# Performance work log

Measured on AMD Instinct MI355X. Metric: run time of the kernel, lower is better.

## Reference

```python
import jax, jax.numpy as jnp
import numpy as np

N, M = 100000, 12          # atoms, neighbors per atom
ORIG, F, NBR, H = 92, 64, 41, 128
NC = 3                     # n_conv
C = 3125                   # crystals
EPS = 1e-5                 # BatchNorm eps (torch default)


def setup_inputs() -> dict:
    key = jax.random.key(0)
    ks = jax.random.split(key, 8)
    w = lambda k, s: jax.random.normal(k, s, jnp.float32) * 0.05
    return {
        "atom_fea": jax.random.normal(ks[0], (N, ORIG), jnp.float32),
        "nbr_fea": jax.random.normal(ks[1], (N, M, NBR), jnp.float32),
        "nbr_fea_idx": jax.random.randint(ks[2], (N, M), 0, N),
        "seg_ids": jnp.sort(jax.random.randint(ks[3], (N,), 0, C)),
        "n_crystals": C,
        "mask": jnp.ones((ORIG,), jnp.float32),
        "embW": w(ks[4], (ORIG, F)), "embb": jnp.zeros((F,), jnp.float32),
        "fcW": w(ks[5], (NC, 2 * F + NBR, 2 * F)), "fcb": jnp.zeros((NC, 2 * F), jnp.float32),
        "bn1g": jnp.ones((NC, 2 * F), jnp.float32), "bn1b": jnp.zeros((NC, 2 * F), jnp.float32),
        "bn2g": jnp.ones((NC, F), jnp.float32), "bn2b": jnp.zeros((NC, F), jnp.float32),
        "c2fW": w(ks[6], (F, H)), "c2fb": jnp.zeros((H,), jnp.float32),
        "outW": w(ks[7], (H, 1)), "outb": jnp.zeros((1,), jnp.float32),
    }


def _bn(x, g, b):
    # BatchNorm1d in training mode: biased batch stats over dim 0
    mu = x.mean(0)
    var = x.var(0)
    return (x - mu) * jax.lax.rsqrt(var + EPS) * g + b


def reference(atom_fea, nbr_fea, nbr_fea_idx, seg_ids, n_crystals, mask,
              embW, embb, fcW, fcb, bn1g, bn1b, bn2g, bn2b,
              c2fW, c2fb, outW, outb):
    x = (atom_fea * mask) @ embW + embb              # [N, F]
    for l in range(NC):                              # fixed small layer loop
        nbr = x[nbr_fea_idx]                         # [N, M, F] gather
        self_f = jnp.broadcast_to(x[:, None, :], (N, M, F))
        tot = jnp.concatenate([self_f, nbr, nbr_fea], axis=-1)   # [N, M, 2F+NBR]
        g = tot @ fcW[l] + fcb[l]                    # [N, M, 2F]
        g = _bn(g.reshape(N * M, 2 * F), bn1g[l], bn1b[l]).reshape(N, M, 2 * F)
        filt, core = g[..., :F], g[..., F:]
        summed = jnp.sum(jax.nn.sigmoid(filt) * jax.nn.softplus(core), axis=1)  # [N, F]
        x = jax.nn.softplus(x + _bn(summed, bn2g[l], bn2b[l]))
    # per-crystal mean pooling (segment ids replace list of index maps)
    sums = jax.ops.segment_sum(x, seg_ids, num_segments=n_crystals)
    cnt = jax.ops.segment_sum(jnp.ones((N,), x.dtype), seg_ids, num_segments=n_crystals)
    crys = sums / jnp.maximum(cnt, 1.0)[:, None]     # [C, F]
    crys = jax.nn.softplus(jax.nn.softplus(crys) @ c2fW + c2fb)  # [C, H]
    return crys @ outW + outb                        # [C, 1]
```

## Files before the change

kernel.cpp:

```cpp
#include <hip/hip_runtime.h>
#include <hip/hip_bf16.h>


#define NN    100000
#define MM    12
#define ORIG  92
#define FF    64
#define NBR   41
#define HH    128
#define NCONV 3
#define CC    3125
#define K2    169
#define GG    128
#define EPSV  1e-5f

#define TILE_ATOMS 8
#define TILE_ROWS  96
#define NTILES     (NN / TILE_ATOMS)
#define SLOTS      24
#define WPK_L      (48 * 64 * 8)
#define CONV_GRID  1024
#define ETILES     1563
#define PCHUNK_ROWS 128
#define PCHUNK_F32  (PCHUNK_ROWS * NBR)
#define PCHUNK_U4   (PCHUNK_F32 / 4)
#define NPCHUNK     ((NN * MM) / PCHUNK_ROWS)
#define LOG2E_F    1.44269504088896341f
#define LN2_F      0.69314718055994531f

typedef __attribute__((ext_vector_type(8))) short bf16x8;
typedef __attribute__((ext_vector_type(4))) float f32x4;

__device__ __forceinline__ float softplusf(float v) {
    return fmaxf(v, 0.f) + log1pf(expf(-fabsf(v)));
}
__device__ __forceinline__ float sigmoidf_(float v) {
    return 1.f / (1.f + expf(-v));
}
__device__ __forceinline__ ushort f2bf(float f) {
    __hip_bfloat16 h = __float2bfloat16(f);
    return *(ushort*)&h;
}
__device__ __forceinline__ float bf2f(ushort h) {
    uint u = ((uint)h) << 16;
    return __uint_as_float(u);
}
__device__ __forceinline__ void gload_lds16(const void* gsrc, void* ldst) {
    __builtin_amdgcn_global_load_lds(
        (const __attribute__((address_space(1))) unsigned int*)gsrc,
        (__attribute__((address_space(3))) unsigned int*)ldst, 16, 0, 0);
}

__global__ void packWemb_kernel(const float* __restrict__ embW, const float* __restrict__ mask,
                                ushort* __restrict__ wemb) {
    int b = blockIdx.x;
    int cf = b / 3;
    int kk = b - cf * 3;
    int lane = threadIdx.x;
    int c = cf * 16 + (lane & 15);
#pragma unroll
    for (int i = 0; i < 8; i++) {
        int k = kk * 32 + (lane >> 4) * 8 + i;
        float v = (k < ORIG) ? mask[k] * embW[k * FF + c] : 0.f;
        wemb[((size_t)b * 64 + lane) * 8 + i] = f2bf(v);
    }
}

__launch_bounds__(256)
__global__ void embed_mfma(const float* __restrict__ af, const ushort* __restrict__ wemb,
                           const float* __restrict__ embb,
                           float* __restrict__ x, ushort* __restrict__ xb) {
    __shared__ __align__(16) ushort Ae[64 * 128];
    const int t = threadIdx.x;
    const int lane = t & 63;
    const int w = t >> 6;
    const int l15 = lane & 15;
    const int lg = lane >> 4;
    const int a0 = blockIdx.x * 64;

    bf16x8 bfrag[4][3];
#pragma unroll
    for (int cf = 0; cf < 4; cf++)
#pragma unroll
        for (int kk = 0; kk < 3; kk++)
            bfrag[cf][kk] = *(const bf16x8*)&wemb[(((size_t)(cf * 3 + kk)) * 64 + lane) * 8];

#pragma unroll
    for (int uu = 0; uu < 3; uu++) {
        int u = uu * 256 + t;
        int row = u / 12;
        int slot = u - row * 12;
        int a = a0 + row;
        if (a >= NN) a = NN - 1;
        const float* src = af + (size_t)a * ORIG + slot * 8;
        float v[8];
        float4 p0 = *(const float4*)src;
        v[0] = p0.x; v[1] = p0.y; v[2] = p0.z; v[3] = p0.w;
        if (slot < 11) {
            float4 p1 = *(const float4*)(src + 4);
            v[4] = p1.x; v[5] = p1.y; v[6] = p1.z; v[7] = p1.w;
        } else {
            v[4] = v[5] = v[6] = v[7] = 0.f;
        }
        uint4 val;
        val.x = (uint)f2bf(v[0]) | ((uint)f2bf(v[1]) << 16);
        val.y = (uint)f2bf(v[2]) | ((uint)f2bf(v[3]) << 16);
        val.z = (uint)f2bf(v[4]) | ((uint)f2bf(v[5]) << 16);
        val.w = (uint)f2bf(v[6]) | ((uint)f2bf(v[7]) << 16);
        *(uint4*)&Ae[row * 128 + ((slot ^ (row & 7)) * 8)] = val;
    }
    __syncthreads();

    f32x4 acc[4];
#pragma unroll
    for (int cf = 0; cf < 4; cf++) acc[cf] = (f32x4){0.f, 0.f, 0.f, 0.f};

#pragma unroll
    for (int kk = 0; kk < 3; kk++) {
        int row = w * 16 + l15;
        int slot = kk * 4 + lg;
        bf16x8 a = *(const bf16x8*)&Ae[row * 128 + ((slot ^ (row & 7)) * 8)];
#pragma unroll
        for (int cf = 0; cf < 4; cf++)
            acc[cf] = __builtin_amdgcn_mfma_f32_16x16x32_bf16(a, bfrag[cf][kk], acc[cf], 0, 0, 0);
    }

#pragma unroll
    for (int cf = 0; cf < 4; cf++) {
        int c = cf * 16 + l15;
        float bb = embb[c];
#pragma unroll
        for (int q = 0; q < 4; q++) {
            int a = a0 + w * 16 + lg * 4 + q;
            if (a < NN) {
                float v = acc[cf][q] + bb;
                x[(size_t)a * FF + c] = v;
                xb[(size_t)a * FF + c] = f2bf(v);
            }
        }
    }
}

__global__ void packW_kernel(const float* __restrict__ fcW, ushort* __restrict__ wpk) {
    int b = blockIdx.x;
    int l = b / 48;
    int r = b - l * 48;
    int cf = r / 6;
    int kk = r - cf * 6;
    int lane = threadIdx.x;
    int c = cf * 16 + (lane & 15);
#pragma unroll
    for (int i = 0; i < 8; i++) {
        int k = kk * 32 + (lane >> 4) * 8 + i;
        float v = (k < K2) ? fcW[(l * K2 + k) * GG + c] : 0.f;
        wpk[((size_t)b * 64 + lane) * 8 + i] = f2bf(v);
    }
}

__launch_bounds__(256)
__global__ void prepack_nbr(const float* __restrict__ nbr_fea, ushort* __restrict__ nbrb) {
    __shared__ float buf[PCHUNK_F32];
    const int t = threadIdx.x;
    for (int chunk = blockIdx.x; chunk < NPCHUNK; chunk += gridDim.x) {
        const uint4* src = (const uint4*)(nbr_fea + (size_t)chunk * PCHUNK_F32);
        __syncthreads();
#pragma unroll
        for (int i = 0; i < 6; i++) {
            int u = i * 256 + t;
            if (u < PCHUNK_U4) *(uint4*)&buf[u * 4] = src[u];
        }
        __syncthreads();
#pragma unroll
        for (int i = 0; i < 4; i++) {
            int u = i * 256 + t;
            int row = u >> 3;
            int kb = (u & 7) * 8;
            ushort h[8];
#pragma unroll
            for (int j = 0; j < 8; j++)
                h[j] = (kb + j < NBR) ? f2bf(buf[row * NBR + kb + j]) : (ushort)0;
            uint4 val;
            val.x = (uint)h[0] | ((uint)h[1] << 16);
            val.y = (uint)h[2] | ((uint)h[3] << 16);
            val.z = (uint)h[4] | ((uint)h[5] << 16);
            val.w = (uint)h[6] | ((uint)h[7] << 16);
            *(uint4*)&nbrb[((size_t)chunk * PCHUNK_ROWS + row) * 64 + kb] = val;
        }
    }
}

template <int MODE>
__launch_bounds__(256, 3)
__global__ void conv_fused(const ushort* __restrict__ xb, const ushort* __restrict__ nbrb,
                           const int* __restrict__ nidx, const ushort* __restrict__ wpk_l,
                           const float* __restrict__ fcb_l,
                           float* __restrict__ stats,
                           const float* __restrict__ sc1, const float* __restrict__ sh1,
                           float* __restrict__ summed, float* __restrict__ stats2) {
    __shared__ __align__(16) ushort As[3][TILE_ROWS * 64];
    __shared__ int nbstage[2][TILE_ROWS];
    __shared__ float red[256];

    const int t = threadIdx.x;
    const int lane = t & 63;
    const int w = t >> 6;
    const int l15 = lane & 15;
    const int lg = lane >> 4;

    bf16x8 bfrag[2][6];
#pragma unroll
    for (int c2 = 0; c2 < 2; c2++)
#pragma unroll
        for (int kk = 0; kk < 6; kk++)
            bfrag[c2][kk] = *(const bf16x8*)&wpk_l[((((w + 4 * c2) * 6 + kk) * 64 + lane) * 8)];

    const int chF = w * 16 + l15;
    float scF = 0.f, shF = 0.f, scC = 0.f, shC = 0.f;
    if (MODE == 1) {
        scF = sc1[chF]; shF = sh1[chF];
        scC = sc1[chF + 64]; shC = sh1[chF + 64];
    }

    float sAF = 0.f, sBF = 0.f, sAC = 0.f, sBC = 0.f;
    float s2a = 0.f, s2b = 0.f;

    int pt = t; if (pt >= TILE_ROWS) pt -= TILE_ROWS; if (pt >= TILE_ROWS) pt -= TILE_ROWS;
    const int pidx = (pt & 7) * MM + (pt >> 3);

    int rowi[3], sli[3];
#pragma unroll
    for (int i = 0; i < 3; i++) {
        int u = w * 192 + i * 64 + lane;
        rowi[i] = u >> 3;
        sli[i] = (u & 7) ^ (rowi[i] & 7);
    }
    const ushort* p0p[3];
    const ushort* p2p[3];
#pragma unroll
    for (int i = 0; i < 3; i++) {
        p0p[i] = xb + ((size_t)blockIdx.x * TILE_ATOMS + (rowi[i] & 7)) * 64 + sli[i] * 8;
        p2p[i] = nbrb + ((size_t)blockIdx.x * TILE_ROWS + (rowi[i] & 7) * MM + (rowi[i] >> 3)) * 64
                 + sli[i] * 8;
    }
    const size_t st0 = (size_t)CONV_GRID * TILE_ATOMS * 64;
    const size_t st2 = (size_t)CONV_GRID * TILE_ROWS * 64;

    auto issue0 = [&]() {
#pragma unroll
        for (int i = 0; i < 3; i++) {
            gload_lds16(p0p[i], &As[0][(w * 192 + i * 64) * 8]);
            p0p[i] += st0;
        }
    };
    auto issue1 = [&](int nb) {
#pragma unroll
        for (int i = 0; i < 3; i++)
            gload_lds16(xb + (size_t)nbstage[nb][rowi[i]] * 64 + sli[i] * 8,
                        &As[1][(w * 192 + i * 64) * 8]);
    };
    auto issue2 = [&]() {
#pragma unroll
        for (int i = 0; i < 3; i++) {
            gload_lds16(p2p[i], &As[2][(w * 192 + i * 64) * 8]);
            p2p[i] += st2;
        }
    };

    int tile = blockIdx.x;
    int idx_cur;
    {
        int nx0 = nidx[tile * TILE_ROWS + pidx];
        int nx1 = nidx[(tile + CONV_GRID) * TILE_ROWS + pidx];
        if (t < TILE_ROWS) { nbstage[0][t] = nx0; nbstage[1][t] = nx1; }
        __syncthreads();
        idx_cur = nidx[(tile + 2 * CONV_GRID) * TILE_ROWS + pidx];
        issue0(); issue1(0); issue2();
        asm volatile("" ::: "memory");
    }

    for (int it = 0; tile < NTILES; tile += CONV_GRID, ++it) {
        const bool have1 = (tile + CONV_GRID)     < NTILES;
        const bool have2 = (tile + 2 * CONV_GRID) < NTILES;
        const bool have3 = (tile + 3 * CONV_GRID) < NTILES;

        int idx_next = 0;
        if (have3) idx_next = nidx[(tile + 3 * CONV_GRID) * TILE_ROWS + pidx];

        f32x4 acc[6][2];
#pragma unroll
        for (int rf = 0; rf < 6; rf++)
#pragma unroll
            for (int c2 = 0; c2 < 2; c2++) acc[rf][c2] = (f32x4){0.f, 0.f, 0.f, 0.f};

        if (it == 0)       { asm volatile("s_waitcnt vmcnt(7)"  ::: "memory"); }
        else if (have3) {
            if (MODE == 1) { asm volatile("s_waitcnt vmcnt(11)" ::: "memory"); }
            else           { asm volatile("s_waitcnt vmcnt(7)"  ::: "memory"); }
        } else {
            if (MODE == 1) { asm volatile("s_waitcnt vmcnt(10)" ::: "memory"); }
            else           { asm volatile("s_waitcnt vmcnt(6)"  ::: "memory"); }
        }
        __builtin_amdgcn_s_barrier();
        __builtin_amdgcn_sched_barrier(0);
#pragma unroll
        for (int kx = 0; kx < 2; kx++) {
            int kk = kx;
#pragma unroll
            for (int rf = 0; rf < 6; rf++) {
                int row = rf * 16 + l15;
                int s8r = kx * 4 + lg;
                bf16x8 a = *(const bf16x8*)&As[0][row * 64 + ((s8r ^ (row & 7)) * 8)];
                acc[rf][0] = __builtin_amdgcn_mfma_f32_16x16x32_bf16(a, bfrag[0][kk], acc[rf][0], 0, 0, 0);
                acc[rf][1] = __builtin_amdgcn_mfma_f32_16x16x32_bf16(a, bfrag[1][kk], acc[rf][1], 0, 0, 0);
            }
        }
        asm volatile("" ::: "memory");
        __builtin_amdgcn_s_barrier();
        if (have1) issue0();
        asm volatile("" ::: "memory");

        if (it == 0)       { asm volatile("s_waitcnt vmcnt(7)"  ::: "memory"); }
        else if (!have1) {
            if (MODE == 1) { asm volatile("s_waitcnt vmcnt(7)"  ::: "memory"); }
            else           { asm volatile("s_waitcnt vmcnt(3)"  ::: "memory"); }
        } else if (have3) {
            if (MODE == 1) { asm volatile("s_waitcnt vmcnt(11)" ::: "memory"); }
            else           { asm volatile("s_waitcnt vmcnt(7)"  ::: "memory"); }
        } else {
            if (MODE == 1) { asm volatile("s_waitcnt vmcnt(10)" ::: "memory"); }
            else           { asm volatile("s_waitcnt vmcnt(6)"  ::: "memory"); }
        }
        __builtin_amdgcn_s_barrier();
        __builtin_amdgcn_sched_barrier(0);
#pragma unroll
        for (int kx = 0; kx < 2; kx++) {
            int kk = 2 + kx;
#pragma unroll
            for (int rf = 0; rf < 6; rf++) {
                int row = rf * 16 + l15;
                int s8r = kx * 4 + lg;
                bf16x8 a = *(const bf16x8*)&As[1][row * 64 + ((s8r ^ (row & 7)) * 8)];
                acc[rf][0] = __builtin_amdgcn_mfma_f32_16x16x32_bf16(a, bfrag[0][kk], acc[rf][0], 0, 0, 0);
                acc[rf][1] = __builtin_amdgcn_mfma_f32_16x16x32_bf16(a, bfrag[1][kk], acc[rf][1], 0, 0, 0);
            }
        }
        asm volatile("" ::: "memory");
        __builtin_amdgcn_s_barrier();
        if (have1) issue1((it + 1) & 1);
        asm volatile("" ::: "memory");

        if (it == 0)            { asm volatile("s_waitcnt vmcnt(7)" ::: "memory"); }
        else if (have1 && have3){ asm volatile("s_waitcnt vmcnt(7)" ::: "memory"); }
        else if (have1)         { asm volatile("s_waitcnt vmcnt(6)" ::: "memory"); }
        else                    { asm volatile("s_waitcnt vmcnt(0)" ::: "memory"); }
        __builtin_amdgcn_s_barrier();
        __builtin_amdgcn_sched_barrier(0);
#pragma unroll
        for (int kx = 0; kx < 2; kx++) {
            int kk = 4 + kx;
#pragma unroll
            for (int rf = 0; rf < 6; rf++) {
                int row = rf * 16 + l15;
                int s8r = kx * 4 + lg;
                bf16x8 a = *(const bf16x8*)&As[2][row * 64 + ((s8r ^ (row & 7)) * 8)];
                acc[rf][0] = __builtin_amdgcn_mfma_f32_16x16x32_bf16(a, bfrag[0][kk], acc[rf][0], 0, 0, 0);
                acc[rf][1] = __builtin_amdgcn_mfma_f32_16x16x32_bf16(a, bfrag[1][kk], acc[rf][1], 0, 0, 0);
            }
        }

        if (MODE == 0) {
#pragma unroll
            for (int rf = 0; rf < 6; rf++)
#pragma unroll
                for (int q = 0; q < 4; q++) {
                    float a0 = acc[rf][0][q];
                    float a1 = acc[rf][1][q];
                    sAF += a0; sBF = fmaf(a0, a0, sBF);
                    sAC += a1; sBC = fmaf(a1, a1, sBC);
                }
        } else {
            float psum[4] = {0.f, 0.f, 0.f, 0.f};
#pragma unroll
            for (int rf = 0; rf < 6; rf++)
#pragma unroll
                for (int q = 0; q < 4; q++) {
                    float gF = fmaf(acc[rf][0][q], scF, shF);
                    float gC = fmaf(acc[rf][1][q], scC, shC);
                    float sig = __builtin_amdgcn_rcpf(1.f + __builtin_amdgcn_exp2f(-gF));
                    float sp  = fmaxf(gC, 0.f)
                              + __builtin_amdgcn_logf(1.f + __builtin_amdgcn_exp2f(-fabsf(gC)));
                    psum[q] = fmaf(sig, sp, psum[q]);
                }
#pragma unroll
            for (int q = 0; q < 4; q++) {
                psum[q] *= LN2_F;
                psum[q] += __shfl_xor(psum[q], 32, 64);
            }
            if (lg < 2) {
                int atom0 = tile * TILE_ATOMS;
#pragma unroll
                for (int q = 0; q < 4; q++) {
                    int a_loc = (lg & 1) * 4 + q;
                    float sm = psum[q];
                    summed[(size_t)(atom0 + a_loc) * FF + chF] = sm;
                    s2a += sm; s2b += sm * sm;
                }
            }
        }

        if (have2 && t < TILE_ROWS) nbstage[it & 1][t] = idx_cur;
        idx_cur = idx_next;
        asm volatile("s_waitcnt lgkmcnt(0)" ::: "memory");
        __builtin_amdgcn_s_barrier();
        if (have1) issue2();
        asm volatile("" ::: "memory");
    }

    if (MODE == 0) {
        __syncthreads(); red[t] = sAF; __syncthreads();
        if (t < 64) {
            float s = 0.f;
#pragma unroll
            for (int g2 = 0; g2 < 4; g2++) s += red[(t >> 4) * 64 + g2 * 16 + (t & 15)];
            atomicAdd(&stats[t], s);
        }
        __syncthreads(); red[t] = sBF; __syncthreads();
        if (t < 64) {
            float s = 0.f;
#pragma unroll
            for (int g2 = 0; g2 < 4; g2++) s += red[(t >> 4) * 64 + g2 * 16 + (t & 15)];
            atomicAdd(&stats[128 + t], s);
        }
        __syncthreads(); red[t] = sAC; __syncthreads();
        if (t < 64) {
            float s = 0.f;
#pragma unroll
            for (int g2 = 0; g2 < 4; g2++) s += red[(t >> 4) * 64 + g2 * 16 + (t & 15)];
            atomicAdd(&stats[64 + t], s);
        }
        __syncthreads(); red[t] = sBC; __syncthreads();
        if (t < 64) {
            float s = 0.f;
#pragma unroll
            for (int g2 = 0; g2 < 4; g2++) s += red[(t >> 4) * 64 + g2 * 16 + (t & 15)];
            atomicAdd(&stats[192 + t], s);
        }
    } else {
        __syncthreads(); red[t] = s2a; __syncthreads();
        if (t < 64) {
            float s = 0.f;
#pragma unroll
            for (int g2 = 0; g2 < 4; g2++) s += red[(t >> 4) * 64 + g2 * 16 + (t & 15)];
            atomicAdd(&stats2[t], s);
        }
        __syncthreads(); red[t] = s2b; __syncthreads();
        if (t < 64) {
            float s = 0.f;
#pragma unroll
            for (int g2 = 0; g2 < 4; g2++) s += red[(t >> 4) * 64 + g2 * 16 + (t & 15)];
            atomicAdd(&stats2[64 + t], s);
        }
    }
}

template <int PASS>
__launch_bounds__(256, 2)
__global__ void conv_mfma(const ushort* __restrict__ xb, const float* __restrict__ nbr_fea,
                          const int* __restrict__ nidx, const ushort* __restrict__ wpk_l,
                          const float* __restrict__ fcb_l,
                          float* __restrict__ stats,
                          const float* __restrict__ sc1, const float* __restrict__ sh1,
                          float* __restrict__ summed, float* __restrict__ stats2) {
    __shared__ __align__(16) ushort As[TILE_ROWS * 192];
    __shared__ int nb[TILE_ROWS];
    __shared__ float gacc[TILE_ATOMS * FF];
    __shared__ float red[256];

    const int t = threadIdx.x;
    const int lane = t & 63;
    const int w = t >> 6;
    const int l15 = lane & 15;
    const int lg = lane >> 4;

    bf16x8 bfrag[2][6];
#pragma unroll
    for (int c2 = 0; c2 < 2; c2++)
#pragma unroll
        for (int kk = 0; kk < 6; kk++)
            bfrag[c2][kk] = *(const bf16x8*)&wpk_l[((((w + 4 * c2) * 6 + kk) * 64 + lane) * 8)];

    const int chF = w * 16 + l15;
    const int chC = chF + 64;
    const float bF = fcb_l[chF], bC = fcb_l[chC];
    float scF = 0.f, shF = 0.f, scC = 0.f, shC = 0.f;
    if (PASS == 1) { scF = sc1[chF]; shF = sh1[chF]; scC = sc1[chC]; shC = sh1[chC]; }

    float sAF = 0.f, sBF = 0.f, sAC = 0.f, sBC = 0.f;
    float s2a = 0.f, s2b = 0.f;

    for (int tile = blockIdx.x; tile < NTILES; tile += gridDim.x) {
        const int ebase = tile * TILE_ROWS;
        __syncthreads();
        if (t < TILE_ROWS) nb[t] = nidx[ebase + t];
        if (PASS == 1) { gacc[t] = 0.f; gacc[256 + t] = 0.f; }
        __syncthreads();

#pragma unroll
        for (int e = t; e < TILE_ROWS * SLOTS; e += 256) {
            int row = e / SLOTS;
            int slot = e - row * SLOTS;
            uint4 val;
            if (slot < 16) {
                int a = (slot < 8) ? (tile * TILE_ATOMS + row / 12) : nb[row];
                val = *(const uint4*)&xb[a * 64 + (slot & 7) * 8];
            } else {
                int kb = (slot - 16) * 8;
                const float* src = nbr_fea + (size_t)(ebase + row) * NBR + kb;
                ushort h[8];
#pragma unroll
                for (int i = 0; i < 8; i++)
                    h[i] = (kb + i < NBR) ? f2bf(src[i]) : (ushort)0;
                val.x = (uint)h[0] | ((uint)h[1] << 16);
                val.y = (uint)h[2] | ((uint)h[3] << 16);
                val.z = (uint)h[4] | ((uint)h[5] << 16);
                val.w = (uint)h[6] | ((uint)h[7] << 16);
            }
            *(uint4*)&As[row * 192 + ((slot ^ (row & 7)) * 8)] = val;
        }
        __syncthreads();

        f32x4 acc[6][2];
#pragma unroll
        for (int rf = 0; rf < 6; rf++)
#pragma unroll
            for (int c2 = 0; c2 < 2; c2++) acc[rf][c2] = (f32x4){0.f, 0.f, 0.f, 0.f};

#pragma unroll
        for (int kk = 0; kk < 6; kk++) {
#pragma unroll
            for (int rf = 0; rf < 6; rf++) {
                int row = rf * 16 + l15;
                int slot = kk * 4 + lg;
                bf16x8 a = *(const bf16x8*)&As[row * 192 + ((slot ^ (row & 7)) * 8)];
                acc[rf][0] = __builtin_amdgcn_mfma_f32_16x16x32_bf16(a, bfrag[0][kk], acc[rf][0], 0, 0, 0);
                acc[rf][1] = __builtin_amdgcn_mfma_f32_16x16x32_bf16(a, bfrag[1][kk], acc[rf][1], 0, 0, 0);
            }
        }

        if (PASS == 0) {
#pragma unroll
            for (int rf = 0; rf < 6; rf++)
#pragma unroll
                for (int q = 0; q < 4; q++) {
                    float a0 = acc[rf][0][q];
                    float a1 = acc[rf][1][q];
                    sAF += a0; sBF = fmaf(a0, a0, sBF);
                    sAC += a1; sBC = fmaf(a1, a1, sBC);
                }
        } else {
#pragma unroll
            for (int rf = 0; rf < 6; rf++) {
                int r0 = rf * 16 + lg * 4;
                float p = 0.f;
#pragma unroll
                for (int q = 0; q < 4; q++) {
                    float gF = (acc[rf][0][q] + bF) * scF + shF;
                    float gC = (acc[rf][1][q] + bC) * scC + shC;
                    p += sigmoidf_(gF) * softplusf(gC);
                }
                atomicAdd(&gacc[(r0 / 12) * FF + chF], p);
            }
            __syncthreads();
#pragma unroll
            for (int rep = 0; rep < 2; rep++) {
                int idx = rep * 256 + t;
                int a = idx >> 6, c = idx & 63;
                float sm = gacc[idx];
                summed[(tile * TILE_ATOMS + a) * FF + c] = sm;
                s2a += sm; s2b += sm * sm;
            }
        }
    }

    if (PASS == 0) {
        __syncthreads(); red[t] = sAF; __syncthreads();
        if (t < 64) {
            float s = 0.f;
#pragma unroll
            for (int g2 = 0; g2 < 4; g2++) s += red[(t >> 4) * 64 + g2 * 16 + (t & 15)];
            atomicAdd(&stats[t], s);
        }
        __syncthreads(); red[t] = sBF; __syncthreads();
        if (t < 64) {
            float s = 0.f;
#pragma unroll
            for (int g2 = 0; g2 < 4; g2++) s += red[(t >> 4) * 64 + g2 * 16 + (t & 15)];
            atomicAdd(&stats[128 + t], s);
        }
        __syncthreads(); red[t] = sAC; __syncthreads();
        if (t < 64) {
            float s = 0.f;
#pragma unroll
            for (int g2 = 0; g2 < 4; g2++) s += red[(t >> 4) * 64 + g2 * 16 + (t & 15)];
            atomicAdd(&stats[64 + t], s);
        }
        __syncthreads(); red[t] = sBC; __syncthreads();
        if (t < 64) {
            float s = 0.f;
#pragma unroll
            for (int g2 = 0; g2 < 4; g2++) s += red[(t >> 4) * 64 + g2 * 16 + (t & 15)];
            atomicAdd(&stats[192 + t], s);
        }
    } else {
        __syncthreads(); red[t] = s2a; __syncthreads();
        if (t < 64) {
            float s = red[t] + red[64 + t] + red[128 + t] + red[192 + t];
            atomicAdd(&stats2[t], s);
        }
        __syncthreads(); red[t] = s2b; __syncthreads();
        if (t < 64) {
            float s = red[t] + red[64 + t] + red[128 + t] + red[192 + t];
            atomicAdd(&stats2[64 + t], s);
        }
    }
}

__global__ void fin1_kernel(const float* __restrict__ stats, const float* __restrict__ fcb_l,
                            const float* __restrict__ g, const float* __restrict__ b,
                            float* __restrict__ sc, float* __restrict__ sh, int fold) {
    int c = threadIdx.x;
    const float inv = 1.f / (float)(NN * MM);
    float bia = fcb_l[c];
    float Sa = stats[c], Sb = stats[128 + c];
    float mu = Sa * inv + bia;
    float ex2 = (Sb + 2.f * bia * Sa) * inv + bia * bia;
    float var = ex2 - mu * mu;
    float s = rsqrtf(var + EPSV) * g[c];
    float scv = s;
    float shv = b[c] - mu * s;
    if (fold) { scv *= LOG2E_F; shv *= LOG2E_F; }
    sc[c] = scv;
    sh[c] = shv;
}

__global__ void fin2_kernel(const float* __restrict__ stats2, const float* __restrict__ g,
                            const float* __restrict__ b, float* __restrict__ sc, float* __restrict__ sh) {
    int c = threadIdx.x;
    const float inv = 1.f / (float)NN;
    float mu = stats2[c] * inv;
    float var = stats2[64 + c] * inv - mu * mu;
    float s = rsqrtf(var + EPSV) * g[c];
    sc[c] = s;
    sh[c] = b[c] - mu * s;
}

__global__ void update_x_kernel(float* __restrict__ x, ushort* __restrict__ xb,
                                const float* __restrict__ summed,
                                const float* __restrict__ sc2, const float* __restrict__ sh2) {
    for (int idx = blockIdx.x * blockDim.x + threadIdx.x; idx < NN * FF;
         idx += gridDim.x * blockDim.x) {
        int c = idx & 63;
        float v = softplusf(x[idx] + summed[idx] * sc2[c] + sh2[c]);
        x[idx] = v;
        xb[idx] = f2bf(v);
    }
}

__global__ void update_x_pool_kernel(const float* __restrict__ x,
                                     const float* __restrict__ summed,
                                     const float* __restrict__ sc2, const float* __restrict__ sh2,
                                     const int* __restrict__ seg,
                                     float* __restrict__ csum, float* __restrict__ ccnt) {
    for (int idx = blockIdx.x * blockDim.x + threadIdx.x; idx < NN * FF;
         idx += gridDim.x * blockDim.x) {
        int i = idx >> 6;
        int c = idx & 63;
        float v = softplusf(x[idx] + summed[idx] * sc2[c] + sh2[c]);
        atomicAdd(&csum[seg[i] * FF + c], v);
        if (c == 0) atomicAdd(&ccnt[seg[i]], 1.f);
    }
}

__global__ void head_kernel(const float* __restrict__ csum, const float* __restrict__ ccnt,
                            const float* __restrict__ c2fW, const float* __restrict__ c2fb,
                            const float* __restrict__ outW, const float* __restrict__ outb,
                            float* __restrict__ out) {
    __shared__ float pl[FF];
    __shared__ float red[HH];
    int c = blockIdx.x;
    int t = threadIdx.x;
    if (t < FF) {
        float cnt = fmaxf(ccnt[c], 1.f);
        pl[t] = softplusf(csum[c * FF + t] / cnt);
    }
    __syncthreads();
    float acc = c2fb[t];
    for (int f = 0; f < FF; f++) acc += pl[f] * c2fW[f * HH + t];
    red[t] = softplusf(acc) * outW[t];
    __syncthreads();
    for (int s = 64; s > 0; s >>= 1) {
        if (t < s) red[t] += red[t + s];
        __syncthreads();
    }
    if (t == 0) out[c] = red[0] + outb[0];
}

extern "C" void kernel_launch(void* const* d_in, const int* in_sizes, int n_in,
                              void* d_out, int out_size, void* d_ws, size_t ws_size,
                              hipStream_t stream) {
    const float* atom_fea = (const float*)d_in[0];
    const float* nbr_fea  = (const float*)d_in[1];
    const int*   nbr_idx  = (const int*)d_in[2];
    const int*   seg      = (const int*)d_in[3];
    const float* mask = (const float*)d_in[5];
    const float* embW = (const float*)d_in[6];
    const float* embb = (const float*)d_in[7];
    const float* fcW  = (const float*)d_in[8];
    const float* fcb  = (const float*)d_in[9];
    const float* bn1g = (const float*)d_in[10];
    const float* bn1b = (const float*)d_in[11];
    const float* bn2g = (const float*)d_in[12];
    const float* bn2b = (const float*)d_in[13];
    const float* c2fW = (const float*)d_in[14];
    const float* c2fb = (const float*)d_in[15];
    const float* outW = (const float*)d_in[16];
    const float* outb = (const float*)d_in[17];
    float* out = (float*)d_out;

    float* ws     = (float*)d_ws;
    float* x      = ws;
    float* summed = x + NN * FF;
    float* csum   = summed + NN * FF;
    float* ccnt   = csum + CC * FF;
    float* stats  = ccnt + 3128;
    float* stats2 = stats + 256;
    float* sc1    = stats2 + 128;
    float* sh1    = sc1 + 128;
    float* sc2    = sh1 + 128;
    float* sh2    = sc2 + 64;
    ushort* xb    = (ushort*)(sh2 + 64);
    ushort* wpk   = xb + NN * FF;
    ushort* wemb  = wpk + 3 * WPK_L;
    ushort* nbrb  = wemb + 8192;

    const size_t need_full =
        (size_t)((char*)(nbrb + (size_t)NN * MM * 64) - (char*)d_ws);
    const bool full = (ws_size >= need_full);

    packW_kernel<<<144, 64, 0, stream>>>(fcW, wpk);
    packWemb_kernel<<<12, 64, 0, stream>>>(embW, mask, wemb);
    embed_mfma<<<ETILES, 256, 0, stream>>>(atom_fea, wemb, embb, x, xb);
    if (full) prepack_nbr<<<2048, 256, 0, stream>>>(nbr_fea, nbrb);
    hipMemsetAsync(csum, 0, (CC * FF + CC) * sizeof(float), stream);

    for (int l = 0; l < NCONV; l++) {
        const ushort* wpk_l = wpk + l * WPK_L;
        hipMemsetAsync(stats, 0, (256 + 128) * sizeof(float), stream);
        if (full) {
            conv_fused<0><<<CONV_GRID, 256, 0, stream>>>(xb, nbrb, nbr_idx, wpk_l,
                                                         fcb + l * GG, stats,
                                                         nullptr, nullptr, nullptr, nullptr);
            fin1_kernel<<<1, 128, 0, stream>>>(stats, fcb + l * GG,
                                               bn1g + l * GG, bn1b + l * GG, sc1, sh1, 1);
            conv_fused<1><<<CONV_GRID, 256, 0, stream>>>(xb, nbrb, nbr_idx, wpk_l,
                                                         fcb + l * GG, nullptr,
                                                         sc1, sh1, summed, stats2);
        } else {
            conv_mfma<0><<<2048, 256, 0, stream>>>(xb, nbr_fea, nbr_idx, wpk_l, fcb + l * GG,
                                                   stats, nullptr, nullptr, nullptr, nullptr);
            fin1_kernel<<<1, 128, 0, stream>>>(stats, fcb + l * GG,
                                               bn1g + l * GG, bn1b + l * GG, sc1, sh1, 0);
            conv_mfma<1><<<2048, 256, 0, stream>>>(xb, nbr_fea, nbr_idx, wpk_l, fcb + l * GG,
                                                   nullptr, sc1, sh1, summed, stats2);
        }
        fin2_kernel<<<1, 64, 0, stream>>>(stats2, bn2g + l * FF, bn2b + l * FF, sc2, sh2);
        if (l < NCONV - 1) {
            update_x_kernel<<<2048, 256, 0, stream>>>(x, xb, summed, sc2, sh2);
        } else {
            update_x_pool_kernel<<<2048, 256, 0, stream>>>(x, summed, sc2, sh2,
                                                           seg, csum, ccnt);
        }
    }

    head_kernel<<<CC, 128, 0, stream>>>(csum, ccnt, c2fW, c2fb, outW, outb, out);
}
```

Before: 848.3 us.

## Merge first two K-slab stages and shrink conv grid to 750 blocks

```diff
diff --git a/kernel.cpp b/kernel.cpp
--- a/kernel.cpp
+++ b/kernel.cpp
@@ -19,7 +19,7 @@
 #define NTILES     (NN / TILE_ATOMS)
 #define SLOTS      24
 #define WPK_L      (48 * 64 * 8)
-#define CONV_GRID  1024
+#define CONV_GRID  750
 #define ETILES     1563
 #define PCHUNK_ROWS 128
 #define PCHUNK_F32  (PCHUNK_ROWS * NBR)
@@ -292,61 +292,34 @@
 #pragma unroll
             for (int c2 = 0; c2 < 2; c2++) acc[rf][c2] = (f32x4){0.f, 0.f, 0.f, 0.f};
 
-        if (it == 0)       { asm volatile("s_waitcnt vmcnt(7)"  ::: "memory"); }
+        if (it == 0)       { asm volatile("s_waitcnt vmcnt(4)"  ::: "memory"); }
         else if (have3) {
-            if (MODE == 1) { asm volatile("s_waitcnt vmcnt(11)" ::: "memory"); }
-            else           { asm volatile("s_waitcnt vmcnt(7)"  ::: "memory"); }
+            if (MODE == 1) { asm volatile("s_waitcnt vmcnt(8)"  ::: "memory"); }
+            else           { asm volatile("s_waitcnt vmcnt(4)"  ::: "memory"); }
         } else {
-            if (MODE == 1) { asm volatile("s_waitcnt vmcnt(10)" ::: "memory"); }
-            else           { asm volatile("s_waitcnt vmcnt(6)"  ::: "memory"); }
+            if (MODE == 1) { asm volatile("s_waitcnt vmcnt(7)"  ::: "memory"); }
+            else           { asm volatile("s_waitcnt vmcnt(3)"  ::: "memory"); }
         }
         __builtin_amdgcn_s_barrier();
         __builtin_amdgcn_sched_barrier(0);
 #pragma unroll
-        for (int kx = 0; kx < 2; kx++) {
-            int kk = kx;
-#pragma unroll
-            for (int rf = 0; rf < 6; rf++) {
-                int row = rf * 16 + l15;
-                int s8r = kx * 4 + lg;
-                bf16x8 a = *(const bf16x8*)&As[0][row * 64 + ((s8r ^ (row & 7)) * 8)];
-                acc[rf][0] = __builtin_amdgcn_mfma_f32_16x16x32_bf16(a, bfrag[0][kk], acc[rf][0], 0, 0, 0);
-                acc[rf][1] = __builtin_amdgcn_mfma_f32_16x16x32_bf16(a, bfrag[1][kk], acc[rf][1], 0, 0, 0);
+        for (int sb = 0; sb < 2; sb++) {
+#pragma unroll
+            for (int kx = 0; kx < 2; kx++) {
+                int kk = sb * 2 + kx;
+#pragma unroll
+                for (int rf = 0; rf < 6; rf++) {
+                    int row = rf * 16 + l15;
+                    int s8r = kx * 4 + lg;
+                    bf16x8 a = *(const bf16x8*)&As[sb][row * 64 + ((s8r ^ (row & 7)) * 8)];
+                    acc[rf][0] = __builtin_amdgcn_mfma_f32_16x16x32_bf16(a, bfrag[0][kk], acc[rf][0], 0, 0, 0);
+                    acc[rf][1] = __builtin_amdgcn_mfma_f32_16x16x32_bf16(a, bfrag[1][kk], acc[rf][1], 0, 0, 0);
+                }
             }
         }
         asm volatile("" ::: "memory");
         __builtin_amdgcn_s_barrier();
-        if (have1) issue0();
-        asm volatile("" ::: "memory");
-
-        if (it == 0)       { asm volatile("s_waitcnt vmcnt(7)"  ::: "memory"); }
-        else if (!have1) {
-            if (MODE == 1) { asm volatile("s_waitcnt vmcnt(7)"  ::: "memory"); }
-            else           { asm volatile("s_waitcnt vmcnt(3)"  ::: "memory"); }
-        } else if (have3) {
-            if (MODE == 1) { asm volatile("s_waitcnt vmcnt(11)" ::: "memory"); }
-            else           { asm volatile("s_waitcnt vmcnt(7)"  ::: "memory"); }
-        } else {
-            if (MODE == 1) { asm volatile("s_waitcnt vmcnt(10)" ::: "memory"); }
-            else           { asm volatile("s_waitcnt vmcnt(6)"  ::: "memory"); }
-        }
-        __builtin_amdgcn_s_barrier();
-        __builtin_amdgcn_sched_barrier(0);
-#pragma unroll
-        for (int kx = 0; kx < 2; kx++) {
-            int kk = 2 + kx;
-#pragma unroll
-            for (int rf = 0; rf < 6; rf++) {
-                int row = rf * 16 + l15;
-                int s8r = kx * 4 + lg;
-                bf16x8 a = *(const bf16x8*)&As[1][row * 64 + ((s8r ^ (row & 7)) * 8)];
-                acc[rf][0] = __builtin_amdgcn_mfma_f32_16x16x32_bf16(a, bfrag[0][kk], acc[rf][0], 0, 0, 0);
-                acc[rf][1] = __builtin_amdgcn_mfma_f32_16x16x32_bf16(a, bfrag[1][kk], acc[rf][1], 0, 0, 0);
-            }
-        }
-        asm volatile("" ::: "memory");
-        __builtin_amdgcn_s_barrier();
-        if (have1) issue1((it + 1) & 1);
+        if (have1) { issue0(); issue1((it + 1) & 1); }
         asm volatile("" ::: "memory");
 
         if (it == 0)            { asm volatile("s_waitcnt vmcnt(7)" ::: "memory"); }
```

New measurement: 715.8 us (median of 2 runs). 15.6% less time.
